# Performance work log

Hardware: AMD Instinct MI355X
Metric: run time of the kernel (lower is better)

Reference implementation:

```python
import jax, jax.numpy as jnp
import numpy as np

N_NODES = 200000  # graph size
D = 128           # feature dim == out_size
N1 = 81920        # layer-1 node set size
B = 8192          # batch size
K = 10            # num_sample neighbors


def setup_inputs() -> dict:
    key = jax.random.key(0)
    k = jax.random.split(key, 7)
    raw_features = jax.random.normal(k[0], (N_NODES, D), dtype=jnp.float32)
    # xavier-like scale for weights [out, 2*in]
    W1 = jax.random.normal(k[1], (D, 2 * D), dtype=jnp.float32) * (1.0 / np.sqrt(2 * D))
    W2 = jax.random.normal(k[2], (D, 2 * D), dtype=jnp.float32) * (1.0 / np.sqrt(2 * D))
    layer1_nodes = jax.random.randint(k[3], (N1,), 0, N_NODES)
    neigh0_idx = jax.random.randint(k[4], (N1, K), 0, N_NODES)
    map_batch = jax.random.randint(k[5], (B,), 0, N1)
    neigh1_idx = jax.random.randint(k[6], (B, K), 0, N1)
    return {
        "raw_features": raw_features,
        "W1": W1,
        "W2": W2,
        "layer1_nodes": layer1_nodes,
        "neigh0_idx": neigh0_idx,
        "map_batch": map_batch,
        "neigh1_idx": neigh1_idx,
    }


def _sage_layer(self_feats, agg_feats, W):
    # combined = cat([self, agg], dim=1); relu(W @ combined.T).T == relu(combined @ W.T)
    combined = jnp.concatenate([self_feats, agg_feats], axis=1)
    return jax.nn.relu(combined @ W.T)


def reference(raw_features, W1, W2, layer1_nodes, neigh0_idx, map_batch, neigh1_idx):
    # Layer 1: aggregate raw features over K sampled neighbors (MEAN), gcn=False
    agg0 = jnp.mean(raw_features[neigh0_idx], axis=1)        # [N1, D]
    self0 = raw_features[layer1_nodes]                        # [N1, D]
    h1 = _sage_layer(self0, agg0, W1)                         # [N1, D]
    # Layer 2: aggregate layer-1 embeddings for the batch nodes
    agg1 = jnp.mean(h1[neigh1_idx], axis=1)                   # [B, D]
    self1 = h1[map_batch]                                     # [B, D]
    h2 = _sage_layer(self1, agg1, W2)                         # [B, D]
    return h2
```

## Files before the change

kernel.cpp:

```cpp
#include <hip/hip_runtime.h>
#include <stdint.h>

#define D 128
#define K_NEI 10
#define TILE_M 64

typedef __bf16 bf16x8 __attribute__((ext_vector_type(8)));
typedef float f32x4 __attribute__((ext_vector_type(4)));

__device__ __forceinline__ uint32_t f2bf(float f) {
    union { float f; uint32_t u; } v; v.f = f;
    uint32_t u = v.u;
    return (u + 0x7FFFu + ((u >> 16) & 1u)) >> 16;
}
__device__ __forceinline__ float bf2f(uint32_t h) {
    union { uint32_t u; float f; } v; v.u = h << 16; return v.f;
}
__device__ __forceinline__ uint32_t pack2(float a, float b) {
    return f2bf(a) | (f2bf(b) << 16);
}
__device__ __forceinline__ bf16x8 u4_as_bf16x8(uint4 u) {
    union { uint4 u; bf16x8 b; } v; v.u = u; return v.b;
}
__device__ __forceinline__ uint2 cvt4(f32x4 v) {
    union { __bf16 b[4]; uint2 u; } o;
    o.b[0] = (__bf16)v[0]; o.b[1] = (__bf16)v[1];
    o.b[2] = (__bf16)v[2]; o.b[3] = (__bf16)v[3];
    return o.u;
}
__device__ __forceinline__ bf16x8 cvt8(f32x4 lo, f32x4 hi) {
    union { __bf16 b[8]; bf16x8 v; } o;
    o.b[0] = (__bf16)lo[0]; o.b[1] = (__bf16)lo[1];
    o.b[2] = (__bf16)lo[2]; o.b[3] = (__bf16)lo[3];
    o.b[4] = (__bf16)hi[0]; o.b[5] = (__bf16)hi[1];
    o.b[6] = (__bf16)hi[2]; o.b[7] = (__bf16)hi[3];
    return o.v;
}

__global__ void convert_Wc(const float* __restrict__ W1, const float* __restrict__ W2,
                           uint16_t* __restrict__ O1, uint16_t* __restrict__ O2)
{
    const float* W = (blockIdx.x < 16) ? W1 : W2;
    uint16_t*    O = (blockIdx.x < 16) ? O1 : O2;
    int t = (blockIdx.x & 15) * 256 + threadIdx.x;
    const float s = (t & 16) ? 0.1f : 1.0f;
    const float* src = W + (size_t)t * 8;
    f32x4 a = *(const f32x4*)src * s;
    f32x4 b = *(const f32x4*)(src + 4) * s;
    uint2 lo = cvt4(a), hi = cvt4(b);
    uint4 o; o.x = lo.x; o.y = lo.y; o.z = hi.x; o.w = hi.y;
    *(uint4*)(O + (size_t)t * 8) = o;
}

template <bool SRC_F32, bool OUT_F32>
__global__ __launch_bounds__(256)
void sage_fused(const void* __restrict__ src_,
                const uint16_t* __restrict__ Wc,
                const int* __restrict__ self_idx,
                const int* __restrict__ neigh_idx,
                void* __restrict__ out_, int M)
{
    const int tid  = threadIdx.x;
    const int lane = tid & 63;
    const int r16  = lane & 15;
    const int q    = lane >> 4;
    const int g    = blockIdx.x * 64 + (tid >> 6) * 16 + r16;

    const int2* nrow2 = (const int2*)(neigh_idx + (size_t)g * K_NEI);
    int idx[K_NEI];
    #pragma unroll
    for (int k = 0; k < 5; ++k) {
        int2 p = nrow2[k];
        idx[2 * k] = p.x; idx[2 * k + 1] = p.y;
    }
    const int self = self_idx[g];

    bf16x8 a[8];
    f32x4 agg[8];
    #pragma unroll
    for (int x = 0; x < 8; ++x) agg[x] = (f32x4){0.f, 0.f, 0.f, 0.f};

    if (SRC_F32) {
        const float* src  = (const float*)src_;
        const float* srow = src + (size_t)self * D + q * 8;
        #pragma unroll
        for (int ks = 0; ks < 4; ++ks)
            a[ks] = cvt8(*(const f32x4*)(srow + ks * 32),
                         *(const f32x4*)(srow + ks * 32 + 4));
        #pragma unroll
        for (int k = 0; k < K_NEI; ++k) {
            const float* r = src + (size_t)idx[k] * D + q * 8;
            #pragma unroll
            for (int ks = 0; ks < 4; ++ks) {
                agg[2 * ks]     += *(const f32x4*)(r + ks * 32);
                agg[2 * ks + 1] += *(const f32x4*)(r + ks * 32 + 4);
            }
        }
    } else {
        const uint16_t* src = (const uint16_t*)src_;
        #pragma unroll
        for (int ks = 0; ks < 4; ++ks)
            a[ks] = u4_as_bf16x8(*(const uint4*)(src + (size_t)self * D + q * 8 + ks * 32));
        #pragma unroll
        for (int k = 0; k < K_NEI; ++k) {
            const uint16_t* r = src + (size_t)idx[k] * D + q * 8;
            #pragma unroll
            for (int ks = 0; ks < 4; ++ks) {
                uint4 v = *(const uint4*)(r + ks * 32);
                agg[2 * ks]     += (f32x4){bf2f(v.x & 0xFFFFu), bf2f(v.x >> 16),
                                           bf2f(v.y & 0xFFFFu), bf2f(v.y >> 16)};
                agg[2 * ks + 1] += (f32x4){bf2f(v.z & 0xFFFFu), bf2f(v.z >> 16),
                                           bf2f(v.w & 0xFFFFu), bf2f(v.w >> 16)};
            }
        }
    }
    #pragma unroll
    for (int ks = 0; ks < 4; ++ks)
        a[4 + ks] = cvt8(agg[2 * ks], agg[2 * ks + 1]);

    f32x4 acc[8];
    #pragma unroll
    for (int nt = 0; nt < 8; ++nt) acc[nt] = (f32x4){0.f, 0.f, 0.f, 0.f};

    const uint16_t* wb = Wc + (size_t)r16 * 256 + q * 8;
    #pragma unroll
    for (int nt = 0; nt < 8; ++nt)
        #pragma unroll
        for (int ks = 0; ks < 8; ++ks) {
            bf16x8 w = *(const bf16x8*)(wb + (size_t)nt * 16 * 256 + ks * 32);
            acc[nt] = __builtin_amdgcn_mfma_f32_16x16x32_bf16(w, a[ks], acc[nt], 0, 0, 0);
        }

    #pragma unroll
    for (int nt = 0; nt < 8; ++nt) {
        f32x4 v = acc[nt];
        v[0] = v[0] > 0.f ? v[0] : 0.f;
        v[1] = v[1] > 0.f ? v[1] : 0.f;
        v[2] = v[2] > 0.f ? v[2] : 0.f;
        v[3] = v[3] > 0.f ? v[3] : 0.f;
        const int col = nt * 16 + q * 4;
        if (OUT_F32)
            *(f32x4*)((float*)out_ + (size_t)g * D + col) = v;
        else
            *(uint2*)((uint16_t*)out_ + (size_t)g * D + col) = cvt4(v);
    }
}

template <bool FEATS_F32, bool OUT_F32>
__global__ void sage_layer(const void* __restrict__ feats_,
                           const float* __restrict__ W,
                           const int* __restrict__ self_idx,
                           const int* __restrict__ neigh_idx,
                           void* __restrict__ out_)
{
    __shared__ __align__(16) uint16_t Alds[TILE_M * 128];
    __shared__ __align__(16) uint16_t Wlds[128 * 128];

    const int tid  = threadIdx.x;
    const int wave = tid >> 6;
    const int lane = tid & 63;
    const int r16  = lane & 15;
    const int q    = lane >> 4;
    const int G    = blockIdx.x * TILE_M;

    const float*    feats_f = (const float*)feats_;
    const uint16_t* feats_b = (const uint16_t*)feats_;

    f32x4 acc[8];
    #pragma unroll
    for (int nt = 0; nt < 8; ++nt) acc[nt] = (f32x4){0.f, 0.f, 0.f, 0.f};

    for (int half = 0; half < 2; ++half) {
        #pragma unroll
        for (int it = 0; it < 8; ++it) {
            int t = it * 256 + tid;
            int j = t >> 4, c = t & 15;
            const float* src = W + (size_t)j * 256 + half * 128 + c * 8;
            f32x4 w0 = *(const f32x4*)(src);
            f32x4 w1 = *(const f32x4*)(src + 4);
            uint4 o;
            o.x = pack2(w0[0], w0[1]); o.y = pack2(w0[2], w0[3]);
            o.z = pack2(w1[0], w1[1]); o.w = pack2(w1[2], w1[3]);
            int cs = c ^ (j & 15);
            *(uint4*)(Wlds + j * 128 + cs * 8) = o;
        }
        if (half == 0) {
            #pragma unroll
            for (int it = 0; it < 4; ++it) {
                int t = it * 256 + tid;
                int n = t >> 4, c = t & 15;
                int node = self_idx[G + n];
                uint4 o;
                if (FEATS_F32) {
                    const float* src = feats_f + (size_t)node * D + c * 8;
                    f32x4 f0 = *(const f32x4*)(src);
                    f32x4 f1 = *(const f32x4*)(src + 4);
                    o.x = pack2(f0[0], f0[1]); o.y = pack2(f0[2], f0[3]);
                    o.z = pack2(f1[0], f1[1]); o.w = pack2(f1[2], f1[3]);
                } else {
                    o = *(const uint4*)(feats_b + (size_t)node * D + c * 8);
                }
                int cs = c ^ (n & 15);
                *(uint4*)(Alds + n * 128 + cs * 8) = o;
            }
        } else {
            #pragma unroll
            for (int it = 0; it < 4; ++it) {
                int t = it * 256 + tid;
                int n = t >> 4, c = t & 15;
                const int* nrow = neigh_idx + (size_t)(G + n) * K_NEI;
                float s0=0,s1=0,s2=0,s3=0,s4=0,s5=0,s6=0,s7=0;
                #pragma unroll
                for (int k = 0; k < K_NEI; ++k) {
                    if (FEATS_F32) {
                        const float* src = feats_f + (size_t)nrow[k] * D + c * 8;
                        f32x4 f0 = *(const f32x4*)(src);
                        f32x4 f1 = *(const f32x4*)(src + 4);
                        s0 += f0[0]; s1 += f0[1]; s2 += f0[2]; s3 += f0[3];
                        s4 += f1[0]; s5 += f1[1]; s6 += f1[2]; s7 += f1[3];
                    } else {
                        uint4 v = *(const uint4*)(feats_b + (size_t)nrow[k] * D + c * 8);
                        s0 += bf2f(v.x & 0xFFFFu); s1 += bf2f(v.x >> 16);
                        s2 += bf2f(v.y & 0xFFFFu); s3 += bf2f(v.y >> 16);
                        s4 += bf2f(v.z & 0xFFFFu); s5 += bf2f(v.z >> 16);
                        s6 += bf2f(v.w & 0xFFFFu); s7 += bf2f(v.w >> 16);
                    }
                }
                const float inv = 0.1f;
                uint4 o;
                o.x = pack2(s0 * inv, s1 * inv);
                o.y = pack2(s2 * inv, s3 * inv);
                o.z = pack2(s4 * inv, s5 * inv);
                o.w = pack2(s6 * inv, s7 * inv);
                int cs = c ^ (n & 15);
                *(uint4*)(Alds + n * 128 + cs * 8) = o;
            }
        }
        __syncthreads();

        #pragma unroll
        for (int ks = 0; ks < 4; ++ks) {
            int cidx = ks * 4 + q;
            bf16x8 a = *(const bf16x8*)(Alds + (wave * 16 + r16) * 128 + ((cidx ^ r16) * 8));
            bf16x8 b[8];
            #pragma unroll
            for (int nt = 0; nt < 8; ++nt) {
                int jj = nt * 16 + r16;
                b[nt] = *(const bf16x8*)(Wlds + jj * 128 + ((cidx ^ r16) * 8));
            }
            #pragma unroll
            for (int nt = 0; nt < 8; ++nt)
                acc[nt] = __builtin_amdgcn_mfma_f32_16x16x32_bf16(a, b[nt], acc[nt], 0, 0, 0);
        }
        __syncthreads();
    }

    const int row_base = G + wave * 16 + q * 4;
    #pragma unroll
    for (int nt = 0; nt < 8; ++nt) {
        int col = nt * 16 + r16;
        #pragma unroll
        for (int r = 0; r < 4; ++r) {
            float v = acc[nt][r];
            v = v > 0.f ? v : 0.f;
            if (OUT_F32) ((float*)out_)[(size_t)(row_base + r) * D + col] = v;
            else ((uint16_t*)out_)[(size_t)(row_base + r) * D + col] = (uint16_t)f2bf(v);
        }
    }
}

extern "C" void kernel_launch(void* const* d_in, const int* in_sizes, int n_in,
                              void* d_out, int out_size, void* d_ws, size_t ws_size,
                              hipStream_t stream) {
    const float* raw = (const float*)d_in[0];
    const float* W1  = (const float*)d_in[1];
    const float* W2  = (const float*)d_in[2];
    const int* layer1_nodes = (const int*)d_in[3];
    const int* neigh0       = (const int*)d_in[4];
    const int* map_batch    = (const int*)d_in[5];
    const int* neigh1       = (const int*)d_in[6];

    const int N1 = in_sizes[3];
    const int B  = in_sizes[5];

    const size_t szH1 = (size_t)N1 * 128 * 2;
    const size_t szW  = 128 * 256 * 2;
    const size_t need = szH1 + 2 * szW;

    if (ws_size >= need && (N1 % 64) == 0 && (B % 64) == 0) {
        uint16_t* h1  = (uint16_t*)d_ws;
        uint16_t* W1c = h1 + (size_t)N1 * 128;
        uint16_t* W2c = W1c + 128 * 256;

        convert_Wc<<<32, 256, 0, stream>>>(W1, W2, W1c, W2c);

        sage_fused<true,  false><<<N1 / 64, 256, 0, stream>>>(raw, W1c, layer1_nodes, neigh0, h1, N1);

        sage_fused<false, true ><<<B  / 64, 256, 0, stream>>>(h1,  W2c, map_batch,    neigh1, d_out, B);
        return;
    }

    uint16_t* h1 = (uint16_t*)d_ws;
    sage_layer<true,  false><<<N1 / TILE_M, 256, 0, stream>>>(raw, W1, layer1_nodes, neigh0, h1);
    sage_layer<false, true ><<<B  / TILE_M, 256, 0, stream>>>(h1,  W2, map_batch,    neigh1, d_out);
}
```

Before: 248.9 us.

## Compute layer-1 embeddings only for nodes referenced by the batch

Adds a mark-and-compact pass that flags every layer-1 node referenced by map_batch or neigh1, builds a list of those nodes with an atomic counter, and runs the layer-1 kernel only over that list. The goal is to skip computing h1 rows that the second layer never reads (at most 90k references into 81920 nodes, so a sizeable fraction goes unused). It also halves the block size to 128 threads and loads neighbour rows two at a time for more memory-level parallelism. The cost is three extra small launches and early-exit blocks whose count is known only on the device.

```diff
diff --git a/kernel.cpp b/kernel.cpp
--- a/kernel.cpp
+++ b/kernel.cpp
@@ -37,34 +37,78 @@
     return o.v;
 }
 
-__global__ void convert_Wc(const float* __restrict__ W1, const float* __restrict__ W2,
-                           uint16_t* __restrict__ O1, uint16_t* __restrict__ O2)
-{
-    const float* W = (blockIdx.x < 16) ? W1 : W2;
-    uint16_t*    O = (blockIdx.x < 16) ? O1 : O2;
-    int t = (blockIdx.x & 15) * 256 + threadIdx.x;
-    const float s = (t & 16) ? 0.1f : 1.0f;
-    const float* src = W + (size_t)t * 8;
-    f32x4 a = *(const f32x4*)src * s;
-    f32x4 b = *(const f32x4*)(src + 4) * s;
-    uint2 lo = cvt4(a), hi = cvt4(b);
-    uint4 o; o.x = lo.x; o.y = lo.y; o.z = hi.x; o.w = hi.y;
-    *(uint4*)(O + (size_t)t * 8) = o;
-}
-
-template <bool SRC_F32, bool OUT_F32>
-__global__ __launch_bounds__(256)
+__global__ void convert_zero(const float* __restrict__ W1, const float* __restrict__ W2,
+                             uint16_t* __restrict__ O1, uint16_t* __restrict__ O2,
+                             int* __restrict__ flags, int* __restrict__ counter, int N1)
+{
+    const int b = blockIdx.x;
+    if (b < 32) {
+        const float* W = (b < 16) ? W1 : W2;
+        uint16_t*    O = (b < 16) ? O1 : O2;
+        int t = (b & 15) * 256 + threadIdx.x;
+        const float s = (t & 16) ? 0.1f : 1.0f;
+        const float* src = W + (size_t)t * 8;
+        f32x4 a = *(const f32x4*)src * s;
+        f32x4 c = *(const f32x4*)(src + 4) * s;
+        uint2 lo = cvt4(a), hi = cvt4(c);
+        uint4 o; o.x = lo.x; o.y = lo.y; o.z = hi.x; o.w = hi.y;
+        *(uint4*)(O + (size_t)t * 8) = o;
+    } else {
+        if (b == 32 && threadIdx.x == 0) *counter = 0;
+        for (int i = (b - 32) * 256 + threadIdx.x; i < N1; i += 160 * 256)
+            flags[i] = 0;
+    }
+}
+
+__global__ void mark_used(const int* __restrict__ map_batch,
+                          const int* __restrict__ neigh1,
+                          int* __restrict__ flags, int B)
+{
+    const int t = blockIdx.x * 256 + threadIdx.x;
+    const int T = B + B * K_NEI;
+    if (t >= T) return;
+    const int idx = (t < B) ? map_batch[t] : neigh1[t - B];
+    flags[idx] = 1;
+}
+
+__global__ void compact_used(const int* __restrict__ flags,
+                             int* __restrict__ list, int* __restrict__ counter, int N1)
+{
+    const int i = blockIdx.x * 256 + threadIdx.x;
+    if (i < N1 && flags[i]) {
+        int p = atomicAdd(counter, 1);
+        list[p] = i;
+    }
+}
+
+template <bool SRC_F32, bool OUT_F32, bool USE_LIST>
+__global__ __launch_bounds__(128)
 void sage_fused(const void* __restrict__ src_,
                 const uint16_t* __restrict__ Wc,
                 const int* __restrict__ self_idx,
                 const int* __restrict__ neigh_idx,
-                void* __restrict__ out_, int M)
+                void* __restrict__ out_, int M,
+                const int* __restrict__ list,
+                const int* __restrict__ cnt_p)
 {
     const int tid  = threadIdx.x;
     const int lane = tid & 63;
     const int r16  = lane & 15;
     const int q    = lane >> 4;
-    const int g    = blockIdx.x * 64 + (tid >> 6) * 16 + r16;
+    const int base = blockIdx.x * 32 + (tid >> 6) * 16;
+
+    int g;
+    if (USE_LIST) {
+        const int cnt = *cnt_p;
+        if (base >= cnt) return;
+        int li = base + r16;
+        if (li >= cnt) li = cnt - 1;
+        g = list[li];
+    } else {
+        g = base + r16;
+        if (base >= M) return;
+        if (g >= M) g = M - 1;
+    }
 
     const int2* nrow2 = (const int2*)(neigh_idx + (size_t)g * K_NEI);
     int idx[K_NEI];
@@ -83,36 +127,60 @@
     if (SRC_F32) {
         const float* src  = (const float*)src_;
         const float* srow = src + (size_t)self * D + q * 8;
+        f32x4 sl[8];
+        #pragma unroll
+        for (int ks = 0; ks < 4; ++ks) {
+            sl[2 * ks]     = *(const f32x4*)(srow + ks * 32);
+            sl[2 * ks + 1] = *(const f32x4*)(srow + ks * 32 + 4);
+        }
+        #pragma unroll
+        for (int kp = 0; kp < 5; ++kp) {
+            const float* r0 = src + (size_t)idx[2 * kp]     * D + q * 8;
+            const float* r1 = src + (size_t)idx[2 * kp + 1] * D + q * 8;
+            f32x4 t[8], u[8];
+            #pragma unroll
+            for (int ks = 0; ks < 4; ++ks) {
+                t[2 * ks]     = *(const f32x4*)(r0 + ks * 32);
+                t[2 * ks + 1] = *(const f32x4*)(r0 + ks * 32 + 4);
+                u[2 * ks]     = *(const f32x4*)(r1 + ks * 32);
+                u[2 * ks + 1] = *(const f32x4*)(r1 + ks * 32 + 4);
+            }
+            #pragma unroll
+            for (int x = 0; x < 8; ++x) agg[x] += t[x] + u[x];
+        }
         #pragma unroll
         for (int ks = 0; ks < 4; ++ks)
-            a[ks] = cvt8(*(const f32x4*)(srow + ks * 32),
-                         *(const f32x4*)(srow + ks * 32 + 4));
-        #pragma unroll
-        for (int k = 0; k < K_NEI; ++k) {
-            const float* r = src + (size_t)idx[k] * D + q * 8;
-            #pragma unroll
-            for (int ks = 0; ks < 4; ++ks) {
-                agg[2 * ks]     += *(const f32x4*)(r + ks * 32);
-                agg[2 * ks + 1] += *(const f32x4*)(r + ks * 32 + 4);
-            }
-        }
+            a[ks] = cvt8(sl[2 * ks], sl[2 * ks + 1]);
     } else {
         const uint16_t* src = (const uint16_t*)src_;
-        #pragma unroll
-        for (int ks = 0; ks < 4; ++ks)
-            a[ks] = u4_as_bf16x8(*(const uint4*)(src + (size_t)self * D + q * 8 + ks * 32));
-        #pragma unroll
-        for (int k = 0; k < K_NEI; ++k) {
-            const uint16_t* r = src + (size_t)idx[k] * D + q * 8;
+        const uint16_t* srow = src + (size_t)self * D + q * 8;
+        uint4 sv[4];
+        #pragma unroll
+        for (int ks = 0; ks < 4; ++ks) sv[ks] = *(const uint4*)(srow + ks * 32);
+        #pragma unroll
+        for (int kp = 0; kp < 5; ++kp) {
+            const uint16_t* r0 = src + (size_t)idx[2 * kp]     * D + q * 8;
+            const uint16_t* r1 = src + (size_t)idx[2 * kp + 1] * D + q * 8;
+            uint4 t[4], u[4];
             #pragma unroll
             for (int ks = 0; ks < 4; ++ks) {
-                uint4 v = *(const uint4*)(r + ks * 32);
-                agg[2 * ks]     += (f32x4){bf2f(v.x & 0xFFFFu), bf2f(v.x >> 16),
-                                           bf2f(v.y & 0xFFFFu), bf2f(v.y >> 16)};
-                agg[2 * ks + 1] += (f32x4){bf2f(v.z & 0xFFFFu), bf2f(v.z >> 16),
-                                           bf2f(v.w & 0xFFFFu), bf2f(v.w >> 16)};
-            }
-        }
+                t[ks] = *(const uint4*)(r0 + ks * 32);
+                u[ks] = *(const uint4*)(r1 + ks * 32);
+            }
+            #pragma unroll
+            for (int ks = 0; ks < 4; ++ks) {
+                agg[2 * ks]     += (f32x4){bf2f(t[ks].x & 0xFFFFu), bf2f(t[ks].x >> 16),
+                                           bf2f(t[ks].y & 0xFFFFu), bf2f(t[ks].y >> 16)};
+                agg[2 * ks + 1] += (f32x4){bf2f(t[ks].z & 0xFFFFu), bf2f(t[ks].z >> 16),
+                                           bf2f(t[ks].w & 0xFFFFu), bf2f(t[ks].w >> 16)};
+                agg[2 * ks]     += (f32x4){bf2f(u[ks].x & 0xFFFFu), bf2f(u[ks].x >> 16),
+                                           bf2f(u[ks].y & 0xFFFFu), bf2f(u[ks].y >> 16)};
+                agg[2 * ks + 1] += (f32x4){bf2f(u[ks].z & 0xFFFFu), bf2f(u[ks].z >> 16),
+                                           bf2f(u[ks].w & 0xFFFFu), bf2f(u[ks].w >> 16)};
+            }
+        }
+        #pragma unroll
+        for (int ks = 0; ks < 4; ++ks) a[ks] = u4_as_bf16x8(sv[ks]);
     }
     #pragma unroll
     for (int ks = 0; ks < 4; ++ks)
@@ -285,18 +353,27 @@
 
     const size_t szH1 = (size_t)N1 * 128 * 2;
     const size_t szW  = 128 * 256 * 2;
-    const size_t need = szH1 + 2 * szW;
-
-    if (ws_size >= need && (N1 % 64) == 0 && (B % 64) == 0) {
-        uint16_t* h1  = (uint16_t*)d_ws;
-        uint16_t* W1c = h1 + (size_t)N1 * 128;
-        uint16_t* W2c = W1c + 128 * 256;
-
-        convert_Wc<<<32, 256, 0, stream>>>(W1, W2, W1c, W2c);
-
-        sage_fused<true,  false><<<N1 / 64, 256, 0, stream>>>(raw, W1c, layer1_nodes, neigh0, h1, N1);
-
-        sage_fused<false, true ><<<B  / 64, 256, 0, stream>>>(h1,  W2c, map_batch,    neigh1, d_out, B);
+    const size_t szAux = (size_t)N1 * 4 * 2 + 64;
+    const size_t need = szH1 + 2 * szW + szAux;
+
+    if (ws_size >= need && (N1 % 16) == 0 && (B % 16) == 0) {
+        uint16_t* h1   = (uint16_t*)d_ws;
+        uint16_t* W1c  = h1 + (size_t)N1 * 128;
+        uint16_t* W2c  = W1c + 128 * 256;
+        int*      flags   = (int*)(W2c + 128 * 256);
+        int*      list    = flags + N1;
+        int*      counter = list + N1;
+
+        convert_zero<<<192, 256, 0, stream>>>(W1, W2, W1c, W2c, flags, counter, N1);
+
+        mark_used<<<(B + B * K_NEI + 255) / 256, 256, 0, stream>>>(map_batch, neigh1, flags, B);
+        compact_used<<<(N1 + 255) / 256, 256, 0, stream>>>(flags, list, counter, N1);
+
+        sage_fused<true,  false, true ><<<(N1 + 31) / 32, 128, 0, stream>>>(
+            raw, W1c, layer1_nodes, neigh0, h1, N1, list, counter);
+
+        sage_fused<false, true,  false><<<(B + 31) / 32, 128, 0, stream>>>(
+            h1, W2c, map_batch, neigh1, d_out, B, nullptr, nullptr);
         return;
     }
 
```

Result: no change. 252.6 us (+1.5%).

## Compute only layer-1 rows needed by the batch and gather from bf16 features

Applied to the files above, without the earlier changes.

A prep kernel converts the whole raw feature table to bf16, converts both weight matrices, and clears a flag array. A mark/compact kernel then uses atomics to build a list of the distinct layer-1 nodes that layer 2 actually references, and layer 1 is evaluated only for those rows. The fused layer kernel is reworked to 16-row tiles. Each thread gathers one 8-element slice, the concatenated self/aggregate rows are staged in a swizzled LDS buffer, and each wave computes a 32-column slice of the output. The aim is to cut gather bandwidth and skip unused h1 rows. In exchange it adds a full-table conversion pass and atomic contention in the compaction step.

```diff
diff --git a/kernel.cpp b/kernel.cpp
--- a/kernel.cpp
+++ b/kernel.cpp
@@ -28,117 +28,151 @@
     o.b[2] = (__bf16)v[2]; o.b[3] = (__bf16)v[3];
     return o.u;
 }
-__device__ __forceinline__ bf16x8 cvt8(f32x4 lo, f32x4 hi) {
-    union { __bf16 b[8]; bf16x8 v; } o;
-    o.b[0] = (__bf16)lo[0]; o.b[1] = (__bf16)lo[1];
-    o.b[2] = (__bf16)lo[2]; o.b[3] = (__bf16)lo[3];
-    o.b[4] = (__bf16)hi[0]; o.b[5] = (__bf16)hi[1];
-    o.b[6] = (__bf16)hi[2]; o.b[7] = (__bf16)hi[3];
-    return o.v;
-}
-
-__global__ void convert_Wc(const float* __restrict__ W1, const float* __restrict__ W2,
-                           uint16_t* __restrict__ O1, uint16_t* __restrict__ O2)
+
+__global__ void prep(const float* __restrict__ raw, int nCvt,
+                     const float* __restrict__ W1, const float* __restrict__ W2,
+                     uint16_t* __restrict__ rawb,
+                     uint16_t* __restrict__ W1c, uint16_t* __restrict__ W2c,
+                     int* __restrict__ flags, int* __restrict__ counter, int N1)
 {
-    const float* W = (blockIdx.x < 16) ? W1 : W2;
-    uint16_t*    O = (blockIdx.x < 16) ? O1 : O2;
-    int t = (blockIdx.x & 15) * 256 + threadIdx.x;
-    const float s = (t & 16) ? 0.1f : 1.0f;
-    const float* src = W + (size_t)t * 8;
-    f32x4 a = *(const f32x4*)src * s;
-    f32x4 b = *(const f32x4*)(src + 4) * s;
-    uint2 lo = cvt4(a), hi = cvt4(b);
-    uint4 o; o.x = lo.x; o.y = lo.y; o.z = hi.x; o.w = hi.y;
-    *(uint4*)(O + (size_t)t * 8) = o;
-}
-
-template <bool SRC_F32, bool OUT_F32>
-__global__ __launch_bounds__(256)
-void sage_fused(const void* __restrict__ src_,
-                const uint16_t* __restrict__ Wc,
-                const int* __restrict__ self_idx,
-                const int* __restrict__ neigh_idx,
-                void* __restrict__ out_, int M)
+    const int b = blockIdx.x;
+    if (b < nCvt) {
+        size_t t = (size_t)b * 256 + threadIdx.x;
+        const float* s = raw + t * 8;
+        f32x4 a = *(const f32x4*)s;
+        f32x4 c = *(const f32x4*)(s + 4);
+        uint2 lo = cvt4(a), hi = cvt4(c);
+        uint4 o; o.x = lo.x; o.y = lo.y; o.z = hi.x; o.w = hi.y;
+        *(uint4*)(rawb + t * 8) = o;
+    } else if (b < nCvt + 32) {
+        const int b2 = b - nCvt;
+        const float* W = (b2 < 16) ? W1 : W2;
+        uint16_t*    O = (b2 < 16) ? W1c : W2c;
+        int t = (b2 & 15) * 256 + threadIdx.x;
+        const float s = (t & 16) ? 0.1f : 1.0f;
+        const float* src = W + (size_t)t * 8;
+        f32x4 a = *(const f32x4*)src * s;
+        f32x4 c = *(const f32x4*)(src + 4) * s;
+        uint2 lo = cvt4(a), hi = cvt4(c);
+        uint4 o; o.x = lo.x; o.y = lo.y; o.z = hi.x; o.w = hi.y;
+        *(uint4*)(O + (size_t)t * 8) = o;
+    } else {
+        const int b3 = b - nCvt - 32;
+        if (b3 == 0 && threadIdx.x == 0) *counter = 0;
+        for (int i = b3 * 256 + threadIdx.x; i < N1; i += 160 * 256)
+            flags[i] = 0;
+    }
+}
+
+__global__ void mark_compact(const int* __restrict__ map_batch,
+                             const int* __restrict__ neigh1,
+                             int* __restrict__ flags,
+                             int* __restrict__ list, int* __restrict__ counter, int B)
 {
+    const int t = blockIdx.x * 256 + threadIdx.x;
+    const int T = B + B * K_NEI;
+    if (t >= T) return;
+    const int idx = (t < B) ? map_batch[t] : neigh1[t - B];
+    if (atomicExch(&flags[idx], 1) == 0) {
+        int p = atomicAdd(counter, 1);
+        list[p] = idx;
+    }
+}
+
+template <bool OUT_F32, bool USE_LIST>
+__global__ __launch_bounds__(256, 4)
+void sage_tile(const uint16_t* __restrict__ src,
+               const uint16_t* __restrict__ Wc,
+               const int* __restrict__ self_idx,
+               const int* __restrict__ neigh_idx,
+               void* __restrict__ out_, int M,
+               const int* __restrict__ list,
+               const int* __restrict__ cnt_p)
+{
+    __shared__ __align__(16) uint16_t Clds[16 * 256];
+
     const int tid  = threadIdx.x;
+    const int base = blockIdx.x * 16;
+    const int cnt  = USE_LIST ? *cnt_p : M;
+    if (base >= cnt) return;
+
+    {
+        const int n = tid >> 4;
+        const int j = tid & 15;
+        int li = base + n; if (li >= cnt) li = cnt - 1;
+        const int g = USE_LIST ? list[li] : li;
+
+        const int2* nrow2 = (const int2*)(neigh_idx + (size_t)g * K_NEI);
+        int idx[K_NEI];
+        #pragma unroll
+        for (int k = 0; k < 5; ++k) {
+            int2 p = nrow2[k];
+            idx[2 * k] = p.x; idx[2 * k + 1] = p.y;
+        }
+        const int self = self_idx[g];
+
+        uint4 sv = *(const uint4*)(src + (size_t)self * D + j * 8);
+
+        f32x4 a0 = (f32x4){0.f, 0.f, 0.f, 0.f};
+        f32x4 a1 = (f32x4){0.f, 0.f, 0.f, 0.f};
+        #pragma unroll
+        for (int h = 0; h < 2; ++h) {
+            uint4 v[5];
+            #pragma unroll
+            for (int k = 0; k < 5; ++k)
+                v[k] = *(const uint4*)(src + (size_t)idx[h * 5 + k] * D + j * 8);
+            #pragma unroll
+            for (int k = 0; k < 5; ++k) {
+                a0 += (f32x4){bf2f(v[k].x & 0xFFFFu), bf2f(v[k].x >> 16),
+                              bf2f(v[k].y & 0xFFFFu), bf2f(v[k].y >> 16)};
+                a1 += (f32x4){bf2f(v[k].z & 0xFFFFu), bf2f(v[k].z >> 16),
+                              bf2f(v[k].w & 0xFFFFu), bf2f(v[k].w >> 16)};
+            }
+        }
+
+        const int cs = j ^ n;
+        *(uint4*)(Clds + n * 256 + cs * 8) = sv;
+        uint2 lo = cvt4(a0), hi = cvt4(a1);
+        uint4 o; o.x = lo.x; o.y = lo.y; o.z = hi.x; o.w = hi.y;
+        *(uint4*)(Clds + n * 256 + (16 + cs) * 8) = o;
+    }
+    __syncthreads();
+
+    const int wave = tid >> 6;
     const int lane = tid & 63;
     const int r16  = lane & 15;
     const int q    = lane >> 4;
-    const int g    = blockIdx.x * 64 + (tid >> 6) * 16 + r16;
-
-    const int2* nrow2 = (const int2*)(neigh_idx + (size_t)g * K_NEI);
-    int idx[K_NEI];
-    #pragma unroll
-    for (int k = 0; k < 5; ++k) {
-        int2 p = nrow2[k];
-        idx[2 * k] = p.x; idx[2 * k + 1] = p.y;
-    }
-    const int self = self_idx[g];
 
     bf16x8 a[8];
-    f32x4 agg[8];
-    #pragma unroll
-    for (int x = 0; x < 8; ++x) agg[x] = (f32x4){0.f, 0.f, 0.f, 0.f};
-
-    if (SRC_F32) {
-        const float* src  = (const float*)src_;
-        const float* srow = src + (size_t)self * D + q * 8;
-        #pragma unroll
-        for (int ks = 0; ks < 4; ++ks)
-            a[ks] = cvt8(*(const f32x4*)(srow + ks * 32),
-                         *(const f32x4*)(srow + ks * 32 + 4));
-        #pragma unroll
-        for (int k = 0; k < K_NEI; ++k) {
-            const float* r = src + (size_t)idx[k] * D + q * 8;
-            #pragma unroll
-            for (int ks = 0; ks < 4; ++ks) {
-                agg[2 * ks]     += *(const f32x4*)(r + ks * 32);
-                agg[2 * ks + 1] += *(const f32x4*)(r + ks * 32 + 4);
-            }
-        }
-    } else {
-        const uint16_t* src = (const uint16_t*)src_;
-        #pragma unroll
-        for (int ks = 0; ks < 4; ++ks)
-            a[ks] = u4_as_bf16x8(*(const uint4*)(src + (size_t)self * D + q * 8 + ks * 32));
-        #pragma unroll
-        for (int k = 0; k < K_NEI; ++k) {
-            const uint16_t* r = src + (size_t)idx[k] * D + q * 8;
-            #pragma unroll
-            for (int ks = 0; ks < 4; ++ks) {
-                uint4 v = *(const uint4*)(r + ks * 32);
-                agg[2 * ks]     += (f32x4){bf2f(v.x & 0xFFFFu), bf2f(v.x >> 16),
-                                           bf2f(v.y & 0xFFFFu), bf2f(v.y >> 16)};
-                agg[2 * ks + 1] += (f32x4){bf2f(v.z & 0xFFFFu), bf2f(v.z >> 16),
-                                           bf2f(v.w & 0xFFFFu), bf2f(v.w >> 16)};
-            }
-        }
-    }
-    #pragma unroll
-    for (int ks = 0; ks < 4; ++ks)
-        a[4 + ks] = cvt8(agg[2 * ks], agg[2 * ks + 1]);
-
-    f32x4 acc[8];
-    #pragma unroll
-    for (int nt = 0; nt < 8; ++nt) acc[nt] = (f32x4){0.f, 0.f, 0.f, 0.f};
-
-    const uint16_t* wb = Wc + (size_t)r16 * 256 + q * 8;
-    #pragma unroll
-    for (int nt = 0; nt < 8; ++nt)
+    #pragma unroll
+    for (int ks = 0; ks < 8; ++ks) {
+        const int c  = ks * 4 + q;
+        const int cs = ((c & 15) ^ r16) | (c & 16);
+        a[ks] = *(const bf16x8*)(Clds + r16 * 256 + cs * 8);
+    }
+
+    f32x4 acc[2];
+    acc[0] = (f32x4){0.f, 0.f, 0.f, 0.f};
+    acc[1] = (f32x4){0.f, 0.f, 0.f, 0.f};
+    const uint16_t* wb = Wc + (size_t)(wave * 32 + r16) * 256 + q * 8;
+    #pragma unroll
+    for (int nt = 0; nt < 2; ++nt)
         #pragma unroll
         for (int ks = 0; ks < 8; ++ks) {
             bf16x8 w = *(const bf16x8*)(wb + (size_t)nt * 16 * 256 + ks * 32);
             acc[nt] = __builtin_amdgcn_mfma_f32_16x16x32_bf16(w, a[ks], acc[nt], 0, 0, 0);
         }
 
-    #pragma unroll
-    for (int nt = 0; nt < 8; ++nt) {
+    int li = base + r16; if (li >= cnt) li = cnt - 1;
+    const int g = USE_LIST ? list[li] : li;
+    #pragma unroll
+    for (int nt = 0; nt < 2; ++nt) {
         f32x4 v = acc[nt];
         v[0] = v[0] > 0.f ? v[0] : 0.f;
         v[1] = v[1] > 0.f ? v[1] : 0.f;
         v[2] = v[2] > 0.f ? v[2] : 0.f;
         v[3] = v[3] > 0.f ? v[3] : 0.f;
-        const int col = nt * 16 + q * 4;
+        const int col = wave * 32 + nt * 16 + q * 4;
         if (OUT_F32)
             *(f32x4*)((float*)out_ + (size_t)g * D + col) = v;
         else
@@ -280,23 +314,37 @@
     const int* map_batch    = (const int*)d_in[5];
     const int* neigh1       = (const int*)d_in[6];
 
+    const int N_NODES = in_sizes[0] / D;
     const int N1 = in_sizes[3];
     const int B  = in_sizes[5];
 
-    const size_t szH1 = (size_t)N1 * 128 * 2;
-    const size_t szW  = 128 * 256 * 2;
-    const size_t need = szH1 + 2 * szW;
-
-    if (ws_size >= need && (N1 % 64) == 0 && (B % 64) == 0) {
-        uint16_t* h1  = (uint16_t*)d_ws;
-        uint16_t* W1c = h1 + (size_t)N1 * 128;
-        uint16_t* W2c = W1c + 128 * 256;
-
-        convert_Wc<<<32, 256, 0, stream>>>(W1, W2, W1c, W2c);
-
-        sage_fused<true,  false><<<N1 / 64, 256, 0, stream>>>(raw, W1c, layer1_nodes, neigh0, h1, N1);
-
-        sage_fused<false, true ><<<B  / 64, 256, 0, stream>>>(h1,  W2c, map_batch,    neigh1, d_out, B);
+    const size_t szRawb = (size_t)N_NODES * 128 * 2;
+    const size_t szH1   = (size_t)N1 * 128 * 2;
+    const size_t szW    = 128 * 256 * 2;
+    const size_t szAux  = (size_t)N1 * 4 * 2 + 64;
+    const size_t need = szRawb + szH1 + 2 * szW + szAux;
+
+    if (ws_size >= need && (N_NODES % 16) == 0) {
+        uint16_t* rawb = (uint16_t*)d_ws;
+        uint16_t* h1   = rawb + (size_t)N_NODES * 128;
+        uint16_t* W1c  = h1 + (size_t)N1 * 128;
+        uint16_t* W2c  = W1c + 128 * 256;
+        int*      flags   = (int*)(W2c + 128 * 256);
+        int*      list    = flags + N1;
+        int*      counter = list + N1;
+
+        const int nCvt = (N_NODES * D) / 2048;
+        prep<<<nCvt + 192, 256, 0, stream>>>(raw, nCvt, W1, W2, rawb, W1c, W2c,
+                                             flags, counter, N1);
+
+        mark_compact<<<(B + B * K_NEI + 255) / 256, 256, 0, stream>>>(
+            map_batch, neigh1, flags, list, counter, B);
+
+        sage_tile<false, true ><<<(N1 + 15) / 16, 256, 0, stream>>>(
+            rawb, W1c, layer1_nodes, neigh0, h1, N1, list, counter);
+
+        sage_tile<true,  false><<<(B + 15) / 16, 256, 0, stream>>>(
+            h1, W2c, map_batch, neigh1, d_out, B, nullptr, nullptr);
         return;
     }
 
```

Result: faster. 232.6 us (-6.5%).
